# Kernel tuning notes

Measured on AMD Instinct MI355X. Metric: run time of the kernel, lower is better.

The kernel has to match this reference:

```python
import jax, jax.numpy as jnp
import numpy as np

NQ = 20  # qubits per block
C64 = jnp.complex64
E0 = jnp.array([1.0 + 0.0j, 0.0 + 0.0j], dtype=C64)
PAULI_Z = jnp.array([[1.0, 0.0], [0.0, -1.0]], dtype=C64)


def rx(t):
    c = jnp.cos(t / 2).astype(C64)
    s = jnp.sin(t / 2).astype(C64)
    return jnp.stack([jnp.stack([c, -1j * s]), jnp.stack([-1j * s, c])])


def ry(t):
    c = jnp.cos(t / 2).astype(C64)
    s = jnp.sin(t / 2).astype(C64)
    return jnp.stack([jnp.stack([c, -s]), jnp.stack([s, c])])


def rz(t):
    e = jnp.exp((-0.5j) * t.astype(C64))  # exp(-i t/2)
    z = 0.0 * e
    return jnp.stack([jnp.stack([e, z]), jnp.stack([z, jnp.conj(e)])])


def apply_1q(psi, op, wire):
    # psi: flat 2**NQ statevector; op: 2x2 on `wire` (axis `wire` of (2,)*NQ view)
    psi = psi.reshape((2,) * NQ)
    psi = jnp.tensordot(op, psi, axes=[[1], [wire]])
    psi = jnp.moveaxis(psi, 0, wire)
    return psi.reshape(-1)


def apply_cnot(psi, c, t):
    psi = psi.reshape((2,) * NQ)
    idx0 = (slice(None),) * c + (slice(0, 1),)
    idx1 = (slice(None),) * c + (slice(1, 2),)
    a0 = psi[idx0]
    a1 = jnp.flip(psi[idx1], axis=t)
    return jnp.concatenate([a0, a1], axis=c).reshape(-1)


def _expect(psi, wire_ops):
    phi = psi
    for w, op in wire_ops:
        phi = apply_1q(phi, op, w)
    return jnp.real(jnp.vdot(psi, phi))


def _circuit(xs, pos_w, l1w, l2w):
    # xs: [16,4,3] angles for one image.
    # Heisenberg-pulled-back layer-2 observables: O_q = U_q^dag Z U_q,
    # U_q = RZ RY RX with layer_2_weights[q].
    Os = []
    for q in range(16):
        U = rz(l2w[q, 2]) @ (ry(l2w[q, 1]) @ rx(l2w[q, 0]))
        Os.append(U.conj().T @ PAULI_Z @ U)
    # Four independent 20-qubit block states after layer 1.
    psis = []
    for b in range(4):
        vecs = []
        for i in range(NQ):
            p = 4 * b + i // 5
            j = i % 5
            if j < 4:  # color qubit: RX,RY,RZ data encoding
                v = rz(xs[p, j, 2]) @ (ry(xs[p, j, 1]) @ (rx(xs[p, j, 0]) @ E0))
            else:  # spatial ancilla: RX,RY
                v = ry(pos_w[p, 1]) @ (rx(pos_w[p, 0]) @ E0)
            # layer-1 local rotations folded into the product state
            v = rz(l1w[i, 2]) @ (ry(l1w[i, 1]) @ (rx(l1w[i, 0]) @ v))
            vecs.append(v)
        psi = vecs[0]
        for v in vecs[1:]:
            psi = (psi[:, None] * v[None, :]).reshape(-1)
        for i in range(NQ):  # layer-1 CNOT ring within the block
            psi = apply_cnot(psi, i, (i + 1) % NQ)
        psis.append(psi)
    # Layer-2 CNOT-ring pullback: Z_{s0} -> Z_{s1..s15}; Z_{sk} -> Z_{s0..sk} (k=1..3).
    Efull = [_expect(psis[b], [(j, Os[4 * b + j]) for j in range(4)]) for b in range(4)]
    e0 = _expect(psis[0], [(j, Os[j]) for j in (1, 2, 3)]) * Efull[1] * Efull[2] * Efull[3]
    e1 = _expect(psis[0], [(0, Os[0]), (1, Os[1])])
    e2 = _expect(psis[0], [(0, Os[0]), (1, Os[1]), (2, Os[2])])
    e3 = Efull[0]
    return jnp.stack([e0, e1, e2, e3])


def setup_inputs() -> dict:
    key = jax.random.key(0)
    k1, k2, k3, k4, k5, k6 = jax.random.split(key, 6)
    B = 8
    return {
        "x": jax.random.normal(k1, (B, 16, 4, 3), dtype=jnp.float32),
        "pos_weights": jax.random.normal(k2, (16, 2), dtype=jnp.float32) * 0.01,
        "layer_1_weights": jax.random.normal(k3, (20, 3), dtype=jnp.float32) * 0.1,
        "layer_2_weights": jax.random.normal(k4, (16, 3), dtype=jnp.float32) * 0.1,
        "head_w": jax.random.normal(k5, (512, 4), dtype=jnp.float32) * 0.5,
        "head_b": jax.random.normal(k6, (512,), dtype=jnp.float32) * 0.1,
    }


def reference(x, pos_weights, layer_1_weights, layer_2_weights, head_w, head_b):
    q = jax.vmap(lambda xs: _circuit(xs, pos_weights, layer_1_weights, layer_2_weights))(x)  # [B,4]
    y = q @ head_w.T + head_b  # [B,512]
    n = jnp.linalg.norm(y, axis=-1, keepdims=True)
    return y / jnp.maximum(n, 1e-12)
```

## Files before the change

kernel.cpp:

```cpp
#include <hip/hip_runtime.h>
#include <math.h>


struct STab {
  unsigned lo[7][128];
  unsigned hi[7][128];
};

constexpr STab make_tab() {
  STab T{};
  const int g_nw[7] = {4, 4, 4, 4, 3, 2, 3};
  const int g_w0[7] = {0, 0, 0, 0, 1, 0, 0};
  for (int g = 0; g < 7; ++g) {
    const int nw = g_nw[g], w0 = g_w0[g];
    int nstr = 1;
    for (int k = 0; k < nw; ++k) nstr *= 3;
    for (int t = 0; t < nstr; ++t) {
      unsigned xm = 0, zm = 0, dg = 0;
      int tt = t;
      for (int k = 0; k < nw; ++k) {
        const int d = tt % 3;
        tt /= 3;
        dg |= (unsigned)d << (2 * k);
        const int w = w0 + k;
        if (d != 2) xm |= 1u << w;
        if (d != 0) zm |= 1u << w;
      }
      unsigned sgn = 0;
      for (int c = 19; c >= 0; --c) {
        const int tq = (c + 1) % 20;
        const unsigned xc = (xm >> c) & 1u, zc = (zm >> c) & 1u;
        const unsigned xt = (xm >> tq) & 1u, zt = (zm >> tq) & 1u;
        sgn ^= xc & zt & (xt ^ zc ^ 1u);
        xm ^= xc << tq;
        zm ^= zt << c;
      }
      T.lo[g][t] = xm | (sgn << 20) | (dg << 21);
      T.hi[g][t] = zm;
    }
  }
  return T;
}

__device__ constexpr STab TAB = make_tab();

__device__ __forceinline__ void fsc(float t, float& s, float& c) {
  const float r = t * 0.15915494309189535f;
  s = __builtin_amdgcn_sinf(r);
  c = __builtin_amdgcn_cosf(r);
}

__device__ __forceinline__ void brx(float t, float& x, float& y, float& z) {
  float s, c; fsc(t, s, c);
  float y2 = c * y - s * z;
  z = s * y + c * z;
  y = y2;
  (void)x;
}
__device__ __forceinline__ void bry(float t, float& x, float& y, float& z) {
  float s, c; fsc(t, s, c);
  float z2 = c * z - s * x;
  x = s * z + c * x;
  z = z2;
  (void)y;
}
__device__ __forceinline__ void brz(float t, float& x, float& y, float& z) {
  float s, c; fsc(t, s, c);
  float x2 = c * x - s * y;
  y = s * x + c * y;
  x = x2;
  (void)z;
}

__global__ __launch_bounds__(512) void qie_kernel(
    const float* __restrict__ x,
    const float* __restrict__ posw,
    const float* __restrict__ l1w,
    const float* __restrict__ l2w,
    const float* __restrict__ hw,
    const float* __restrict__ hb,
    float* __restrict__ out)
{
  const int img = blockIdx.x;
  const int tid = threadIdx.x;
  const int wid = tid >> 6, lane = tid & 63;

  const float hw0 = hw[tid * 4 + 0];
  const float hw1 = hw[tid * 4 + 1];
  const float hw2 = hw[tid * 4 + 2];
  const float hw3 = hw[tid * 4 + 3];
  const float hbb = hb[tid];
  unsigned lo1 = 0, hi1 = 0, lo2 = 0, hi2 = 0;
  if (wid < 7) {
    lo1 = TAB.lo[wid][lane];
    hi1 = TAB.hi[wid][lane];
    lo2 = TAB.lo[wid][lane + 64];
    hi2 = TAB.hi[wid][lane + 64];
  }

  __shared__ float bl[4][20][3];
  __shared__ float nv[16][3];
  __shared__ float eg[7];
  __shared__ float red[8];

  if (tid < 80) {
    const int b = tid / 20, i = tid % 20;
    const int p = 4 * b + i / 5, j = i % 5;
    float nx = 0.f, ny = 0.f, nz = 1.f;
    if (j < 4) {
      const float* a = x + ((img * 16 + p) * 4 + j) * 3;
      brx(a[0], nx, ny, nz);
      bry(a[1], nx, ny, nz);
      brz(a[2], nx, ny, nz);
    } else {
      brx(posw[p * 2 + 0], nx, ny, nz);
      bry(posw[p * 2 + 1], nx, ny, nz);
    }
    brx(l1w[i * 3 + 0], nx, ny, nz);
    bry(l1w[i * 3 + 1], nx, ny, nz);
    brz(l1w[i * 3 + 2], nx, ny, nz);
    bl[b][i][0] = nx; bl[b][i][1] = ny; bl[b][i][2] = nz;
  } else if (tid < 96) {
    const int q = tid - 80;
    float sa, ca, sb, cb;
    fsc(l2w[q * 3 + 0], sa, ca);
    fsc(l2w[q * 3 + 1], sb, cb);
    nv[q][0] = -sb;
    nv[q][1] = sa * cb;
    nv[q][2] = ca * cb;
  }
  __syncthreads();

  float acc = 0.0f;
  if (wid < 7) {
    const int g_nw[7] = {4, 4, 4, 4, 3, 2, 3};
    const int g_qb[7] = {0, 1, 2, 3, 0, 0, 0};
    const int g_w0[7] = {0, 0, 0, 0, 1, 0, 0};
    const int g_ns[7] = {81, 81, 81, 81, 27, 9, 27};
    const int nw = g_nw[wid], qb = g_qb[wid], w0 = g_w0[wid], nstr = g_ns[wid];

    auto eval = [&](unsigned lo, unsigned hi) -> float {
      float coeff = 1.0f;
      const unsigned dg = lo >> 21;
      for (int k = 0; k < nw; ++k)
        coeff *= nv[4 * qb + w0 + k][(dg >> (2 * k)) & 3u];
      float val = ((lo >> 20) & 1u) ? -coeff : coeff;
      const unsigned xm = lo & 0xFFFFFu, zm = hi;
      unsigned um = xm | zm;
      while (um) {
        const int i = __builtin_ctz(um);
        um &= um - 1;
        const unsigned xi = (xm >> i) & 1u, zi = (zm >> i) & 1u;
        val *= bl[qb][i][xi ? (zi ? 1 : 0) : 2];
      }
      return val;
    };

    if (lane < nstr) acc = eval(lo1, hi1);
    if (lane + 64 < nstr) acc += eval(lo2, hi2);
  }
  for (int off = 32; off; off >>= 1) acc += __shfl_xor(acc, off, 64);
  if (wid < 7 && lane == 0) eg[wid] = acc;
  __syncthreads();

  const float q0 = eg[4] * eg[1] * eg[2] * eg[3];
  const float q1 = eg[5];
  const float q2 = eg[6];
  const float q3 = eg[0];

  float y = q0 * hw0 + q1 * hw1 + q2 * hw2 + q3 * hw3 + hbb;
  float ss = y * y;
  for (int off = 32; off; off >>= 1) ss += __shfl_xor(ss, off, 64);
  if (lane == 0) red[wid] = ss;
  __syncthreads();
  const float s = red[0] + red[1] + red[2] + red[3] + red[4] + red[5] + red[6] + red[7];
  const float rn = __builtin_amdgcn_rsqf(fmaxf(s, 1e-24f));
  out[img * 512 + tid] = y * rn;
}

extern "C" void kernel_launch(void* const* d_in, const int* in_sizes, int n_in,
                              void* d_out, int out_size, void* d_ws, size_t ws_size,
                              hipStream_t stream) {
  const float* x    = (const float*)d_in[0];
  const float* posw = (const float*)d_in[1];
  const float* l1w  = (const float*)d_in[2];
  const float* l2w  = (const float*)d_in[3];
  const float* hw   = (const float*)d_in[4];
  const float* hb   = (const float*)d_in[5];
  float* out = (float*)d_out;
  qie_kernel<<<8, 512, 0, stream>>>(x, posw, l1w, l2w, hw, hb, out);
}
```

Before: 10.70 us.

## Compute output norm from precomputed Gram of head weights; use DPP wave reductions

Idle waves (6 of them) precompute the Gram matrix of the head weight columns and bias during the first phase, in parallel with the circuit setup. The output norm is then evaluated as a quadratic form in the four circuit expectations, which removes the final block-wide reduction and one __syncthreads. Shuffle-based wave reductions are replaced with DPP row/broadcast adds. The price is redundant per-block Gram work and a different floating-point summation order for the norm.

```diff
diff --git a/kernel.cpp b/kernel.cpp
--- a/kernel.cpp
+++ b/kernel.cpp
@@ -72,6 +72,21 @@
   (void)z;
 }
 
+template <int CTRL>
+__device__ __forceinline__ float dpp_add(float x) {
+  const int y = __builtin_amdgcn_update_dpp(0, __float_as_int(x), CTRL, 0xF, 0xF, true);
+  return x + __int_as_float(y);
+}
+__device__ __forceinline__ float wave_sum63(float x) {
+  x = dpp_add<0x111>(x);
+  x = dpp_add<0x112>(x);
+  x = dpp_add<0x114>(x);
+  x = dpp_add<0x118>(x);
+  x = dpp_add<0x142>(x);
+  x = dpp_add<0x143>(x);
+  return x;
+}
+
 __global__ __launch_bounds__(512) void qie_kernel(
     const float* __restrict__ x,
     const float* __restrict__ posw,
@@ -101,7 +116,7 @@
   __shared__ float bl[4][20][3];
   __shared__ float nv[16][3];
   __shared__ float eg[7];
-  __shared__ float red[8];
+  __shared__ float gm[15];
 
   if (tid < 80) {
     const int b = tid / 20, i = tid % 20;
@@ -128,10 +143,38 @@
     nv[q][0] = -sb;
     nv[q][1] = sa * cb;
     nv[q][2] = ca * cb;
+  } else if (tid >= 128) {
+    const int wv = wid - 2;
+    const float4* __restrict__ hw4 = (const float4*)hw;
+    float wx[8], wy[8], wz[8], ww[8], wb[8];
+#pragma unroll
+    for (int k = 0; k < 8; ++k) {
+      const int r = lane + 64 * k;
+      const float4 t = hw4[r];
+      wx[k] = t.x; wy[k] = t.y; wz[k] = t.z; ww[k] = t.w;
+      wb[k] = hb[r];
+    }
+    auto dot8 = [](const float (&A)[8], const float (&B)[8]) {
+      float s = 0.f;
+#pragma unroll
+      for (int k = 0; k < 8; ++k) s += A[k] * B[k];
+      return s;
+    };
+#define REDW(v, A, B)                                   \
+  if ((v) % 6 == wv) {                                  \
+    const float _r = wave_sum63(dot8(A, B));            \
+    if (lane == 63) gm[v] = _r;                         \
+  }
+    REDW(0, wx, wx) REDW(1, wx, wy) REDW(2, wx, wz) REDW(3, wx, ww)
+    REDW(4, wy, wy) REDW(5, wy, wz) REDW(6, wy, ww)
+    REDW(7, wz, wz) REDW(8, wz, ww)
+    REDW(9, ww, ww)
+    REDW(10, wx, wb) REDW(11, wy, wb) REDW(12, wz, wb) REDW(13, ww, wb)
+    REDW(14, wb, wb)
+#undef REDW
   }
   __syncthreads();
 
-  float acc = 0.0f;
   if (wid < 7) {
     const int g_nw[7] = {4, 4, 4, 4, 3, 2, 3};
     const int g_qb[7] = {0, 1, 2, 3, 0, 0, 0};
@@ -156,11 +199,12 @@
       return val;
     };
 
+    float acc = 0.0f;
     if (lane < nstr) acc = eval(lo1, hi1);
     if (lane + 64 < nstr) acc += eval(lo2, hi2);
-  }
-  for (int off = 32; off; off >>= 1) acc += __shfl_xor(acc, off, 64);
-  if (wid < 7 && lane == 0) eg[wid] = acc;
+    acc = wave_sum63(acc);
+    if (lane == 63) eg[wid] = acc;
+  }
   __syncthreads();
 
   const float q0 = eg[4] * eg[1] * eg[2] * eg[3];
@@ -168,12 +212,13 @@
   const float q2 = eg[6];
   const float q3 = eg[0];
 
-  float y = q0 * hw0 + q1 * hw1 + q2 * hw2 + q3 * hw3 + hbb;
-  float ss = y * y;
-  for (int off = 32; off; off >>= 1) ss += __shfl_xor(ss, off, 64);
-  if (lane == 0) red[wid] = ss;
-  __syncthreads();
-  const float s = red[0] + red[1] + red[2] + red[3] + red[4] + red[5] + red[6] + red[7];
+  const float y = q0 * hw0 + q1 * hw1 + q2 * hw2 + q3 * hw3 + hbb;
+  const float s =
+      q0 * q0 * gm[0] + q1 * q1 * gm[4] + q2 * q2 * gm[7] + q3 * q3 * gm[9] +
+      2.f * (q0 * (q1 * gm[1] + q2 * gm[2] + q3 * gm[3]) +
+             q1 * (q2 * gm[5] + q3 * gm[6]) + q2 * q3 * gm[8] +
+             q0 * gm[10] + q1 * gm[11] + q2 * gm[12] + q3 * gm[13]) +
+      gm[14];
   const float rn = __builtin_amdgcn_rsqf(fmaxf(s, 1e-24f));
   out[img * 512 + tid] = y * rn;
 }
```

Result: slower. 12.13 us (+13.4%).
